# Kernel tuning notes

Hardware: AMD Instinct MI355X
Metric: run time of the kernel (lower is better)

The kernel has to match this reference:

```python
import jax, jax.numpy as jnp
import numpy as np

NEG_SLOPE = 0.2  # PyG GATConv default


def add_self_loops(edge_index, num_nodes):
    loops = jnp.arange(num_nodes, dtype=edge_index.dtype)
    return jnp.concatenate([edge_index, jnp.stack([loops, loops])], axis=1)


def gat_conv(x, edge_index, W, att_src, att_dst, bias, heads, out_ch, concat):
    # x: [N, F_in]; edge_index: [2, E] with row0=src(j), row1=dst(i)
    N = x.shape[0]
    xl = (x @ W).reshape(N, heads, out_ch)              # [N, H, C]
    src, dst = edge_index[0], edge_index[1]
    a_src = jnp.einsum('nhc,hc->nh', xl, att_src)        # [N, H]
    a_dst = jnp.einsum('nhc,hc->nh', xl, att_dst)        # [N, H]
    alpha = jax.nn.leaky_relu(a_src[src] + a_dst[dst], NEG_SLOPE)  # [E, H]
    # segment softmax over incoming edges of each dst node
    m = jax.ops.segment_max(alpha, dst, num_segments=N)  # [N, H]
    e = jnp.exp(alpha - m[dst])
    denom = jax.ops.segment_sum(e, dst, num_segments=N)
    coef = e / (denom[dst] + 1e-16)                      # [E, H]
    msg = xl[src] * coef[..., None]                      # [E, H, C]
    out = jax.ops.segment_sum(msg, dst, num_segments=N)  # [N, H, C]
    out = out.reshape(N, heads * out_ch) if concat else out.mean(axis=1)
    return out + bias


def setup_inputs() -> dict:
    key = jax.random.key(0)
    ks = jax.random.split(key, 12)
    N, E = 50000, 800000
    nfeat, nhid, nheads, nclass = 512, 8, 8, 16
    hid = nhid * nheads  # 64
    s1 = 1.0 / np.sqrt(nfeat)
    s2 = 1.0 / np.sqrt(hid)
    return {
        'x': jax.random.normal(ks[0], (N, nfeat), jnp.float32),
        'edge_index': jax.random.randint(ks[1], (2, E), 0, N, jnp.int64 if jax.config.jax_enable_x64 else jnp.int32),
        'W1': jax.random.uniform(ks[2], (nfeat, hid), jnp.float32, -s1, s1),
        'att_src1': jax.random.uniform(ks[3], (nheads, nhid), jnp.float32, -s2, s2),
        'att_dst1': jax.random.uniform(ks[4], (nheads, nhid), jnp.float32, -s2, s2),
        'bias1': jnp.zeros((hid,), jnp.float32),
        'W2': jax.random.uniform(ks[5], (hid, nclass), jnp.float32, -s2, s2),
        'att_src2': jax.random.uniform(ks[6], (1, nclass), jnp.float32, -0.25, 0.25),
        'att_dst2': jax.random.uniform(ks[7], (1, nclass), jnp.float32, -0.25, 0.25),
        'bias2': jnp.zeros((nclass,), jnp.float32),
    }


def reference(x, edge_index, W1, att_src1, att_dst1, bias1, W2, att_src2, att_dst2, bias2):
    N = x.shape[0]
    ei = add_self_loops(edge_index, N)
    # dropout layers are identity at inference
    h = gat_conv(x, ei, W1, att_src1, att_dst1, bias1, heads=8, out_ch=8, concat=True)
    o = gat_conv(h, ei, W2, att_src2, att_dst2, bias2, heads=1, out_ch=16, concat=True)
    o = jax.nn.elu(o)
    return jax.nn.log_softmax(o, axis=1)
```

## Files before the change

### kernel.cpp

```cpp
#include <hip/hip_runtime.h>
#include <math.h>

#define NEG_SLOPE 0.2f

typedef short short8 __attribute__((ext_vector_type(8)));
typedef float floatx4 __attribute__((ext_vector_type(4)));

static __device__ __forceinline__ float bf2f(unsigned short u) {
  return __uint_as_float(((unsigned int)u) << 16);
}
static __device__ __forceinline__ unsigned short f2bf(float f) {
  unsigned int u = __float_as_uint(f);
  u = (u + 0x7fffu + ((u >> 16) & 1u)) >> 16;
  return (unsigned short)u;
}
static __device__ __forceinline__ unsigned int pack2(float a, float b) {
  return (unsigned int)f2bf(a) | ((unsigned int)f2bf(b) << 16);
}

__global__ void init_misc(const float* __restrict__ W1, unsigned short* __restrict__ W1t,
                          int* __restrict__ deg, int N) {
  int b = blockIdx.x;
  if (b < 128) {
    int i = b * 256 + threadIdx.x;
    int k = i >> 6, c = i & 63;
    W1t[c * 512 + k] = f2bf(W1[i]);
  } else {
    int n = (b - 128) * 256 + threadIdx.x;
    if (n < N) deg[n] = 1;
  }
}

__global__ __launch_bounds__(256) void gemm1_mfma(const float* __restrict__ A,
                                                  const unsigned short* __restrict__ W1t,
                                                  const float* __restrict__ att_src,
                                                  const float* __restrict__ att_dst,
                                                  unsigned short* __restrict__ xlb,
                                                  float* __restrict__ a_src,
                                                  float* __restrict__ a_dst, int M) {
  __shared__ unsigned short As[64 * 72];
  __shared__ unsigned short Bs[64 * 72];
  int tid = threadIdx.x;
  int w = tid >> 6, lane = tid & 63;
  int q = lane >> 4, cl = lane & 15;
  int row0 = blockIdx.x << 6;
  floatx4 acc[4] = {};

  int sr = tid >> 2;
  int skq = (tid & 3) << 4;
  int arow = row0 + sr;
  bool okA = arow < M;
  const float* Aptr = A + (size_t)arow * 512 + skq;
  const unsigned short* Bptr = W1t + sr * 512 + skq;
  unsigned short* AsW = As + sr * 72 + skq;
  unsigned short* BsW = Bs + sr * 72 + skq;

  float4 ca0 = make_float4(0.f, 0.f, 0.f, 0.f), ca1 = ca0, ca2 = ca0, ca3 = ca0;
  uint4 cb0, cb1;
  if (okA) {
    ca0 = *(const float4*)(Aptr);
    ca1 = *(const float4*)(Aptr + 4);
    ca2 = *(const float4*)(Aptr + 8);
    ca3 = *(const float4*)(Aptr + 12);
  }
  cb0 = *(const uint4*)(Bptr);
  cb1 = *(const uint4*)(Bptr + 8);

#pragma unroll
  for (int k0 = 0; k0 < 512; k0 += 64) {
    __syncthreads();
    uint4 a0, a1;
    a0.x = pack2(ca0.x, ca0.y); a0.y = pack2(ca0.z, ca0.w);
    a0.z = pack2(ca1.x, ca1.y); a0.w = pack2(ca1.z, ca1.w);
    a1.x = pack2(ca2.x, ca2.y); a1.y = pack2(ca2.z, ca2.w);
    a1.z = pack2(ca3.x, ca3.y); a1.w = pack2(ca3.z, ca3.w);
    *(uint4*)(AsW) = a0;
    *(uint4*)(AsW + 8) = a1;
    *(uint4*)(BsW) = cb0;
    *(uint4*)(BsW + 8) = cb1;
    __syncthreads();
    if (k0 < 448) {
      ca0 = make_float4(0.f, 0.f, 0.f, 0.f); ca1 = ca0; ca2 = ca0; ca3 = ca0;
      if (okA) {
        ca0 = *(const float4*)(Aptr + k0 + 64);
        ca1 = *(const float4*)(Aptr + k0 + 68);
        ca2 = *(const float4*)(Aptr + k0 + 72);
        ca3 = *(const float4*)(Aptr + k0 + 76);
      }
      cb0 = *(const uint4*)(Bptr + k0 + 64);
      cb1 = *(const uint4*)(Bptr + k0 + 72);
    }
#pragma unroll
    for (int kk = 0; kk < 2; ++kk) {
      short8 af = *(const short8*)(As + (w * 16 + cl) * 72 + kk * 32 + q * 8);
#pragma unroll
      for (int t = 0; t < 4; ++t) {
        short8 bf = *(const short8*)(Bs + (t * 16 + cl) * 72 + kk * 32 + q * 8);
        acc[t] = __builtin_amdgcn_mfma_f32_16x16x32_bf16(af, bf, acc[t], 0, 0, 0);
      }
    }
  }

  float asv[4], adv[4];
#pragma unroll
  for (int t = 0; t < 4; ++t) {
    asv[t] = att_src[t * 16 + cl];
    adv[t] = att_dst[t * 16 + cl];
  }
#pragma unroll
  for (int reg = 0; reg < 4; ++reg) {
    int r = row0 + w * 16 + q * 4 + reg;
    bool ok = r < M;
#pragma unroll
    for (int t = 0; t < 4; ++t) {
      float v = acc[t][reg];
      if (ok) xlb[(size_t)r * 64 + t * 16 + cl] = f2bf(v);
      float ps = v * asv[t];
      float pd = v * adv[t];
      ps += __shfl_xor(ps, 1); pd += __shfl_xor(pd, 1);
      ps += __shfl_xor(ps, 2); pd += __shfl_xor(pd, 2);
      ps += __shfl_xor(ps, 4); pd += __shfl_xor(pd, 4);
      if (ok && (cl & 7) == 0) {
        int h = t * 2 + (cl >> 3);
        a_src[r * 8 + h] = ps;
        a_dst[r * 8 + h] = pd;
      }
    }
  }
}

__global__ __launch_bounds__(256) void deg_hist_sliced(const int* __restrict__ ei,
                                                       int* __restrict__ deg,
                                                       int E, int N, int ipc) {
  int slice = blockIdx.x & 7;
  int chunk = blockIdx.x >> 3;
  int lo = (int)(((long long)slice * N) >> 3);
  int hi = (int)(((long long)(slice + 1) * N) >> 3);
  int beg = chunk * ipc;
  int end = min(beg + ipc, E);
  for (int i = beg + threadIdx.x; i < end; i += 256) {
    int d = ei[E + i];
    if (d >= lo && d < hi) atomicAdd(&deg[d], 1);
  }
}

__global__ __launch_bounds__(256) void partial_sums(const int* __restrict__ deg,
                                                    int* __restrict__ partials, int N) {
  __shared__ int ws[4];
  int base = blockIdx.x * 512;
  int tid = threadIdx.x;
  int i0 = base + tid * 2;
  int s = 0;
  if (i0 < N) s += deg[i0];
  if (i0 + 1 < N) s += deg[i0 + 1];
#pragma unroll
  for (int off = 32; off >= 1; off >>= 1) s += __shfl_xor(s, off, 64);
  if ((tid & 63) == 0) ws[tid >> 6] = s;
  __syncthreads();
  if (tid == 0) partials[blockIdx.x] = ws[0] + ws[1] + ws[2] + ws[3];
}

__global__ __launch_bounds__(256) void scan_partials(const int* __restrict__ partials,
                                                     int* __restrict__ blockoff,
                                                     int* __restrict__ rowptr, int nb, int N) {
  __shared__ int sums[256];
  int tid = threadIdx.x;
  int chunk = (nb + 255) >> 8;
  int start = tid * chunk, end = min(start + chunk, nb);
  int s = 0;
  for (int i = start; i < end; ++i) s += partials[i];
  sums[tid] = s;
  __syncthreads();
  for (int off = 1; off < 256; off <<= 1) {
    int t = (tid >= off) ? sums[tid - off] : 0;
    __syncthreads();
    sums[tid] += t;
    __syncthreads();
  }
  int run = (tid == 0) ? 0 : sums[tid - 1];
  for (int i = start; i < end; ++i) {
    blockoff[i] = run;
    run += partials[i];
  }
  if (tid == 255) rowptr[N] = sums[255];
}

__global__ __launch_bounds__(256) void scan_blocks(const int* __restrict__ deg,
                                                   const int* __restrict__ blockoff,
                                                   int* __restrict__ rowptr,
                                                   int* __restrict__ cursor, int N) {
  __shared__ int wavesum[4];
  int base = blockIdx.x * 512;
  int tid = threadIdx.x;
  int lane = tid & 63, wv = tid >> 6;
  int i0 = base + tid * 2;
  int d0 = (i0 < N) ? deg[i0] : 0;
  int d1 = (i0 + 1 < N) ? deg[i0 + 1] : 0;
  int s = d0 + d1;
  int v = s;
#pragma unroll
  for (int off = 1; off < 64; off <<= 1) {
    int t = __shfl_up(v, off, 64);
    if (lane >= off) v += t;
  }
  if (lane == 63) wavesum[wv] = v;
  __syncthreads();
  int woff = 0;
  for (int w = 0; w < wv; ++w) woff += wavesum[w];
  int excl = v - s + woff + blockoff[blockIdx.x];
  if (i0 < N) { rowptr[i0] = excl; cursor[i0] = excl; }
  if (i0 + 1 < N) { rowptr[i0 + 1] = excl + d0; cursor[i0 + 1] = excl + d0; }
}

__global__ __launch_bounds__(256) void scatter_sliced(const int* __restrict__ ei,
                                                      int* __restrict__ cursor,
                                                      int* __restrict__ srcs,
                                                      int E, int N, int ipc) {
  int slice = blockIdx.x & 7;
  int chunk = blockIdx.x >> 3;
  int lo = (int)(((long long)slice * N) >> 3);
  int hi = (int)(((long long)(slice + 1) * N) >> 3);
  int total = E + N;
  int beg = chunk * ipc;
  int end = min(beg + ipc, total);
  for (int i = beg + threadIdx.x; i < end; i += 256) {
    int d = (i < E) ? ei[E + i] : (i - E);
    if (d >= lo && d < hi) {
      int s = (i < E) ? ei[i] : d;
      int pos = atomicAdd(&cursor[d], 1);
      srcs[pos] = s;
    }
  }
}

__global__ __launch_bounds__(256) void agg1_csr(const int* __restrict__ rowptr,
                                                const int* __restrict__ srcs,
                                                const float* __restrict__ a_src,
                                                const float* __restrict__ a_dst,
                                                const unsigned short* __restrict__ xlb,
                                                float* __restrict__ agg1, int N) {
  int wave = (blockIdx.x * blockDim.x + threadIdx.x) >> 6;
  int lane = threadIdx.x & 63;
  if (wave >= N) return;
  int half = lane >> 5;
  int j = lane & 31;
  int h = j >> 2;
  int beg = rowptr[wave], end = rowptr[wave + 1];
  float ad = a_dst[wave * 8 + h];
  float den = 0.f, acc0 = 0.f, acc1 = 0.f;
  int p = beg;
  for (; p + 4 <= end; p += 4) {
    int sA = srcs[p + half];
    int sB = srcs[p + 2 + half];
    float aA = a_src[sA * 8 + h] + ad;
    float aB = a_src[sB * 8 + h] + ad;
    ushort2 xA = *(const ushort2*)(xlb + (size_t)sA * 64 + 2 * j);
    ushort2 xB = *(const ushort2*)(xlb + (size_t)sB * 64 + 2 * j);
    aA = aA >= 0.f ? aA : NEG_SLOPE * aA;
    aB = aB >= 0.f ? aB : NEG_SLOPE * aB;
    float wA = __expf(aA), wB = __expf(aB);
    den += wA + wB;
    acc0 += wA * bf2f(xA.x) + wB * bf2f(xB.x);
    acc1 += wA * bf2f(xA.y) + wB * bf2f(xB.y);
  }
  for (; p < end; p += 2) {
    int idx = p + half;
    if (idx < end) {
      int s = srcs[idx];
      float a = a_src[s * 8 + h] + ad;
      ushort2 x = *(const ushort2*)(xlb + (size_t)s * 64 + 2 * j);
      a = a >= 0.f ? a : NEG_SLOPE * a;
      float w = __expf(a);
      den += w;
      acc0 += w * bf2f(x.x);
      acc1 += w * bf2f(x.y);
    }
  }
  den += __shfl_xor(den, 32);
  acc0 += __shfl_xor(acc0, 32);
  acc1 += __shfl_xor(acc1, 32);
  if (half == 0) {
    float inv = 1.f / (den + 1e-16f);
    *(float2*)(agg1 + (size_t)wave * 64 + 2 * j) = make_float2(acc0 * inv, acc1 * inv);
  }
}

__global__ __launch_bounds__(256) void gemm2_prep(const float* __restrict__ agg1,
                                                  const float* __restrict__ bias1,
                                                  const float* __restrict__ W2,
                                                  const float* __restrict__ att_src2,
                                                  const float* __restrict__ att_dst2,
                                                  float* __restrict__ xl2,
                                                  float* __restrict__ a_src2,
                                                  float* __restrict__ a_dst2, int N) {
  __shared__ float hs[16 * 68];
  int tid = threadIdx.x;
  int n0 = blockIdx.x << 4;
  {
    int node = tid >> 4;
    int off = (tid & 15) << 2;
    int nn = n0 + node;
    float4 v = make_float4(0.f, 0.f, 0.f, 0.f);
    if (nn < N) {
      v = *(const float4*)(agg1 + (size_t)nn * 64 + off);
      float4 b = *(const float4*)(bias1 + off);
      v.x += b.x; v.y += b.y; v.z += b.z; v.w += b.w;
    }
    *(float4*)(hs + node * 68 + off) = v;
  }
  __syncthreads();
  int t = tid >> 4, c = tid & 15;
  int n = n0 + t;
  if (n >= N) return;
  float sum = 0.f;
#pragma unroll
  for (int k = 0; k < 64; ++k) sum += hs[t * 68 + k] * W2[k * 16 + c];
  xl2[(size_t)n * 16 + c] = sum;
  float ps = sum * att_src2[c];
  float pd = sum * att_dst2[c];
#pragma unroll
  for (int w = 8; w >= 1; w >>= 1) {
    ps += __shfl_xor(ps, w, 16);
    pd += __shfl_xor(pd, w, 16);
  }
  if (c == 0) {
    a_src2[n] = ps;
    a_dst2[n] = pd;
  }
}

__global__ __launch_bounds__(256) void agg2_fin(const int* __restrict__ rowptr,
                                                const int* __restrict__ srcs,
                                                const float* __restrict__ a_src2,
                                                const float* __restrict__ a_dst2,
                                                const float* __restrict__ xl2,
                                                const float* __restrict__ bias2,
                                                float* __restrict__ out, int N) {
  int t = blockIdx.x * blockDim.x + threadIdx.x;
  int node = t >> 4;
  int c = t & 15;
  if (node >= N) return;
  int beg = rowptr[node], end = rowptr[node + 1];
  float ad = a_dst2[node];
  float den = 0.f, acc = 0.f;
  int p = beg;
  for (; p + 4 <= end; p += 4) {
    int s0 = srcs[p], s1 = srcs[p + 1], s2 = srcs[p + 2], s3 = srcs[p + 3];
    float a0 = a_src2[s0], a1 = a_src2[s1], a2 = a_src2[s2], a3 = a_src2[s3];
    float x0 = xl2[(size_t)s0 * 16 + c], x1 = xl2[(size_t)s1 * 16 + c];
    float x2 = xl2[(size_t)s2 * 16 + c], x3 = xl2[(size_t)s3 * 16 + c];
    a0 += ad; a1 += ad; a2 += ad; a3 += ad;
    a0 = a0 >= 0.f ? a0 : NEG_SLOPE * a0;
    a1 = a1 >= 0.f ? a1 : NEG_SLOPE * a1;
    a2 = a2 >= 0.f ? a2 : NEG_SLOPE * a2;
    a3 = a3 >= 0.f ? a3 : NEG_SLOPE * a3;
    float w0 = __expf(a0), w1 = __expf(a1), w2 = __expf(a2), w3 = __expf(a3);
    den += (w0 + w1) + (w2 + w3);
    acc += w0 * x0 + w1 * x1 + w2 * x2 + w3 * x3;
  }
  for (; p < end; ++p) {
    int s = srcs[p];
    float a = a_src2[s] + ad;
    a = a >= 0.f ? a : NEG_SLOPE * a;
    float w = __expf(a);
    den += w;
    acc += w * xl2[(size_t)s * 16 + c];
  }
  float o = acc / (den + 1e-16f) + bias2[c];
  o = o > 0.f ? o : expm1f(o);
  float mx = o;
#pragma unroll
  for (int w = 8; w >= 1; w >>= 1) mx = fmaxf(mx, __shfl_xor(mx, w, 16));
  float e = __expf(o - mx);
  float ssum = e;
#pragma unroll
  for (int w = 8; w >= 1; w >>= 1) ssum += __shfl_xor(ssum, w, 16);
  out[(size_t)node * 16 + c] = o - mx - logf(ssum);
}

extern "C" void kernel_launch(void* const* d_in, const int* in_sizes, int n_in,
                              void* d_out, int out_size, void* d_ws, size_t ws_size,
                              hipStream_t stream) {
  const float* x        = (const float*)d_in[0];
  const int*   ei       = (const int*)d_in[1];
  const float* W1       = (const float*)d_in[2];
  const float* att_src1 = (const float*)d_in[3];
  const float* att_dst1 = (const float*)d_in[4];
  const float* bias1    = (const float*)d_in[5];
  const float* W2       = (const float*)d_in[6];
  const float* att_src2 = (const float*)d_in[7];
  const float* att_dst2 = (const float*)d_in[8];
  const float* bias2    = (const float*)d_in[9];
  float* out = (float*)d_out;

  int N = in_sizes[0] / 512;
  int E = in_sizes[1] / 2;
  int nb = (N + 511) / 512;

  char* ws = (char*)d_ws;
  unsigned short* xlb = (unsigned short*)ws;        ws += (size_t)N * 64 * 2;
  unsigned short* W1t = (unsigned short*)ws;        ws += (size_t)512 * 64 * 2;
  float* a_src1 = (float*)ws;                       ws += (size_t)N * 8 * 4;
  float* a_dst1 = (float*)ws;                       ws += (size_t)N * 8 * 4;
  float* agg1   = (float*)ws;                       ws += (size_t)N * 64 * 4;
  float* xl2    = (float*)ws;                       ws += (size_t)N * 16 * 4;
  float* a_src2 = (float*)ws;                       ws += (size_t)N * 4;
  float* a_dst2 = (float*)ws;                       ws += (size_t)N * 4;
  int* deg      = (int*)ws;                         ws += (size_t)N * 4;
  int* rowptr   = (int*)ws;                         ws += (size_t)(N + 1) * 4;
  int* cursor   = (int*)ws;                         ws += (size_t)N * 4;
  int* srcs     = (int*)ws;                         ws += (size_t)(E + N) * 4;
  int* partials = (int*)ws;                         ws += (size_t)nb * 4;
  int* blockoff = (int*)ws;                         ws += (size_t)nb * 4;

  init_misc<<<128 + (N + 255) / 256, 256, 0, stream>>>(W1, W1t, deg, N);

  const int NCHUNK = 256;
  int ipc_h = (E + NCHUNK - 1) / NCHUNK;
  int ipc_s = (E + N + NCHUNK - 1) / NCHUNK;
  deg_hist_sliced<<<NCHUNK * 8, 256, 0, stream>>>(ei, deg, E, N, ipc_h);
  partial_sums<<<nb, 256, 0, stream>>>(deg, partials, N);
  scan_partials<<<1, 256, 0, stream>>>(partials, blockoff, rowptr, nb, N);
  scan_blocks<<<nb, 256, 0, stream>>>(deg, blockoff, rowptr, cursor, N);
  scatter_sliced<<<NCHUNK * 8, 256, 0, stream>>>(ei, cursor, srcs, E, N, ipc_s);

  gemm1_mfma<<<(N + 63) / 64, 256, 0, stream>>>(x, W1t, att_src1, att_dst1,
                                                xlb, a_src1, a_dst1, N);
  agg1_csr<<<((size_t)N * 64 + 255) / 256, 256, 0, stream>>>(rowptr, srcs, a_src1, a_dst1,
                                                             xlb, agg1, N);

  gemm2_prep<<<(N + 15) / 16, 256, 0, stream>>>(agg1, bias1, W2, att_src2, att_dst2,
                                                xl2, a_src2, a_dst2, N);
  agg2_fin<<<((size_t)N * 16 + 255) / 256, 256, 0, stream>>>(rowptr, srcs, a_src2, a_dst2,
                                                             xl2, bias2, out, N);
}
```

Before: 325.2 us.

## Fuse degree histogram into GEMM1, single-block scan, fuse agg1 with layer-2 projection

The degree histogram now runs as extra blocks of the GEMM1 launch, so the two independent jobs overlap. The three-kernel prefix scan is replaced by one 1024-thread block that loops over the degree array. Layer-1 aggregation is fused with the layer-2 projection, which removes the agg1 intermediate and its global round trip. Both gather loops are software-pipelined with prefetched source indices. The single-block scan serialises a small amount of work, and the fused aggregation kernel adds shared memory and a per-block W2 load.

```diff
diff --git a/kernel.cpp b/kernel.cpp
--- a/kernel.cpp
+++ b/kernel.cpp
@@ -31,15 +31,32 @@
   }
 }
 
-__global__ __launch_bounds__(256) void gemm1_mfma(const float* __restrict__ A,
+__global__ __launch_bounds__(256) void gemm1_hist(const float* __restrict__ A,
                                                   const unsigned short* __restrict__ W1t,
                                                   const float* __restrict__ att_src,
                                                   const float* __restrict__ att_dst,
                                                   unsigned short* __restrict__ xlb,
                                                   float* __restrict__ a_src,
-                                                  float* __restrict__ a_dst, int M) {
+                                                  float* __restrict__ a_dst, int M,
+                                                  const int* __restrict__ ei,
+                                                  int* __restrict__ deg, int E,
+                                                  int ipc, int G1) {
   __shared__ unsigned short As[64 * 72];
   __shared__ unsigned short Bs[64 * 72];
+  if ((int)blockIdx.x >= G1) {
+    int b = blockIdx.x - G1;
+    int slice = b & 7;
+    int chunk = b >> 3;
+    int lo = (int)(((long long)slice * M) >> 3);
+    int hi = (int)(((long long)(slice + 1) * M) >> 3);
+    int beg = chunk * ipc;
+    int end = min(beg + ipc, E);
+    for (int i = beg + threadIdx.x; i < end; i += 256) {
+      int d = ei[E + i];
+      if (d >= lo && d < hi) atomicAdd(&deg[d], 1);
+    }
+    return;
+  }
   int tid = threadIdx.x;
   int w = tid >> 6, lane = tid & 63;
   int q = lane >> 4, cl = lane & 15;
@@ -129,87 +146,62 @@
   }
 }
 
-__global__ __launch_bounds__(256) void deg_hist_sliced(const int* __restrict__ ei,
-                                                       int* __restrict__ deg,
-                                                       int E, int N, int ipc) {
-  int slice = blockIdx.x & 7;
-  int chunk = blockIdx.x >> 3;
-  int lo = (int)(((long long)slice * N) >> 3);
-  int hi = (int)(((long long)(slice + 1) * N) >> 3);
-  int beg = chunk * ipc;
-  int end = min(beg + ipc, E);
-  for (int i = beg + threadIdx.x; i < end; i += 256) {
-    int d = ei[E + i];
-    if (d >= lo && d < hi) atomicAdd(&deg[d], 1);
-  }
-}
-
-__global__ __launch_bounds__(256) void partial_sums(const int* __restrict__ deg,
-                                                    int* __restrict__ partials, int N) {
-  __shared__ int ws[4];
-  int base = blockIdx.x * 512;
-  int tid = threadIdx.x;
-  int i0 = base + tid * 2;
-  int s = 0;
-  if (i0 < N) s += deg[i0];
-  if (i0 + 1 < N) s += deg[i0 + 1];
-#pragma unroll
-  for (int off = 32; off >= 1; off >>= 1) s += __shfl_xor(s, off, 64);
-  if ((tid & 63) == 0) ws[tid >> 6] = s;
-  __syncthreads();
-  if (tid == 0) partials[blockIdx.x] = ws[0] + ws[1] + ws[2] + ws[3];
-}
-
-__global__ __launch_bounds__(256) void scan_partials(const int* __restrict__ partials,
-                                                     int* __restrict__ blockoff,
-                                                     int* __restrict__ rowptr, int nb, int N) {
-  __shared__ int sums[256];
-  int tid = threadIdx.x;
-  int chunk = (nb + 255) >> 8;
-  int start = tid * chunk, end = min(start + chunk, nb);
-  int s = 0;
-  for (int i = start; i < end; ++i) s += partials[i];
-  sums[tid] = s;
-  __syncthreads();
-  for (int off = 1; off < 256; off <<= 1) {
-    int t = (tid >= off) ? sums[tid - off] : 0;
-    __syncthreads();
-    sums[tid] += t;
-    __syncthreads();
-  }
-  int run = (tid == 0) ? 0 : sums[tid - 1];
-  for (int i = start; i < end; ++i) {
-    blockoff[i] = run;
-    run += partials[i];
-  }
-  if (tid == 255) rowptr[N] = sums[255];
-}
-
-__global__ __launch_bounds__(256) void scan_blocks(const int* __restrict__ deg,
-                                                   const int* __restrict__ blockoff,
-                                                   int* __restrict__ rowptr,
-                                                   int* __restrict__ cursor, int N) {
-  __shared__ int wavesum[4];
-  int base = blockIdx.x * 512;
+__global__ __launch_bounds__(1024) void scan_single(const int* __restrict__ deg,
+                                                    int* __restrict__ rowptr,
+                                                    int* __restrict__ cursor, int N) {
+  __shared__ int wsum[16];
   int tid = threadIdx.x;
   int lane = tid & 63, wv = tid >> 6;
-  int i0 = base + tid * 2;
-  int d0 = (i0 < N) ? deg[i0] : 0;
-  int d1 = (i0 + 1 < N) ? deg[i0 + 1] : 0;
-  int s = d0 + d1;
-  int v = s;
-#pragma unroll
-  for (int off = 1; off < 64; off <<= 1) {
-    int t = __shfl_up(v, off, 64);
-    if (lane >= off) v += t;
-  }
-  if (lane == 63) wavesum[wv] = v;
-  __syncthreads();
-  int woff = 0;
-  for (int w = 0; w < wv; ++w) woff += wavesum[w];
-  int excl = v - s + woff + blockoff[blockIdx.x];
-  if (i0 < N) { rowptr[i0] = excl; cursor[i0] = excl; }
-  if (i0 + 1 < N) { rowptr[i0 + 1] = excl + d0; cursor[i0 + 1] = excl + d0; }
+  int carry = 0;
+  for (int base = 0; base < N; base += 8192) {
+    int i0 = base + tid * 8;
+    int d[8];
+    if (i0 + 8 <= N) {
+      int4 a = *(const int4*)(deg + i0);
+      int4 b = *(const int4*)(deg + i0 + 4);
+      d[0] = a.x; d[1] = a.y; d[2] = a.z; d[3] = a.w;
+      d[4] = b.x; d[5] = b.y; d[6] = b.z; d[7] = b.w;
+    } else {
+#pragma unroll
+      for (int k = 0; k < 8; ++k) d[k] = (i0 + k < N) ? deg[i0 + k] : 0;
+    }
+    int e[8];
+    e[0] = d[0];
+#pragma unroll
+    for (int k = 1; k < 8; ++k) e[k] = e[k - 1] + d[k];
+    int tot = e[7];
+    int v = tot;
+#pragma unroll
+    for (int off = 1; off < 64; off <<= 1) {
+      int t = __shfl_up(v, off, 64);
+      if (lane >= off) v += t;
+    }
+    if (lane == 63) wsum[wv] = v;
+    __syncthreads();
+    int woff = carry;
+    for (int w = 0; w < wv; ++w) woff += wsum[w];
+    int excl = woff + v - tot;
+    int r[8];
+    r[0] = excl;
+#pragma unroll
+    for (int k = 1; k < 8; ++k) r[k] = excl + e[k - 1];
+    if (i0 + 8 <= N) {
+      *(int4*)(rowptr + i0)     = make_int4(r[0], r[1], r[2], r[3]);
+      *(int4*)(rowptr + i0 + 4) = make_int4(r[4], r[5], r[6], r[7]);
+      *(int4*)(cursor + i0)     = make_int4(r[0], r[1], r[2], r[3]);
+      *(int4*)(cursor + i0 + 4) = make_int4(r[4], r[5], r[6], r[7]);
+    } else {
+#pragma unroll
+      for (int k = 0; k < 8; ++k)
+        if (i0 + k < N) { rowptr[i0 + k] = r[k]; cursor[i0 + k] = r[k]; }
+    }
+    int bt = 0;
+#pragma unroll
+    for (int w = 0; w < 16; ++w) bt += wsum[w];
+    carry += bt;
+    __syncthreads();
+  }
+  if (tid == 0) rowptr[N] = carry;
 }
 
 __global__ __launch_bounds__(256) void scatter_sliced(const int* __restrict__ ei,
@@ -233,59 +225,11 @@
   }
 }
 
-__global__ __launch_bounds__(256) void agg1_csr(const int* __restrict__ rowptr,
-                                                const int* __restrict__ srcs,
-                                                const float* __restrict__ a_src,
-                                                const float* __restrict__ a_dst,
-                                                const unsigned short* __restrict__ xlb,
-                                                float* __restrict__ agg1, int N) {
-  int wave = (blockIdx.x * blockDim.x + threadIdx.x) >> 6;
-  int lane = threadIdx.x & 63;
-  if (wave >= N) return;
-  int half = lane >> 5;
-  int j = lane & 31;
-  int h = j >> 2;
-  int beg = rowptr[wave], end = rowptr[wave + 1];
-  float ad = a_dst[wave * 8 + h];
-  float den = 0.f, acc0 = 0.f, acc1 = 0.f;
-  int p = beg;
-  for (; p + 4 <= end; p += 4) {
-    int sA = srcs[p + half];
-    int sB = srcs[p + 2 + half];
-    float aA = a_src[sA * 8 + h] + ad;
-    float aB = a_src[sB * 8 + h] + ad;
-    ushort2 xA = *(const ushort2*)(xlb + (size_t)sA * 64 + 2 * j);
-    ushort2 xB = *(const ushort2*)(xlb + (size_t)sB * 64 + 2 * j);
-    aA = aA >= 0.f ? aA : NEG_SLOPE * aA;
-    aB = aB >= 0.f ? aB : NEG_SLOPE * aB;
-    float wA = __expf(aA), wB = __expf(aB);
-    den += wA + wB;
-    acc0 += wA * bf2f(xA.x) + wB * bf2f(xB.x);
-    acc1 += wA * bf2f(xA.y) + wB * bf2f(xB.y);
-  }
-  for (; p < end; p += 2) {
-    int idx = p + half;
-    if (idx < end) {
-      int s = srcs[idx];
-      float a = a_src[s * 8 + h] + ad;
-      ushort2 x = *(const ushort2*)(xlb + (size_t)s * 64 + 2 * j);
-      a = a >= 0.f ? a : NEG_SLOPE * a;
-      float w = __expf(a);
-      den += w;
-      acc0 += w * bf2f(x.x);
-      acc1 += w * bf2f(x.y);
-    }
-  }
-  den += __shfl_xor(den, 32);
-  acc0 += __shfl_xor(acc0, 32);
-  acc1 += __shfl_xor(acc1, 32);
-  if (half == 0) {
-    float inv = 1.f / (den + 1e-16f);
-    *(float2*)(agg1 + (size_t)wave * 64 + 2 * j) = make_float2(acc0 * inv, acc1 * inv);
-  }
-}
-
-__global__ __launch_bounds__(256) void gemm2_prep(const float* __restrict__ agg1,
+__global__ __launch_bounds__(256) void agg1_fused(const int* __restrict__ rowptr,
+                                                  const int* __restrict__ srcs,
+                                                  const float* __restrict__ a_src,
+                                                  const float* __restrict__ a_dst,
+                                                  const unsigned short* __restrict__ xlb,
                                                   const float* __restrict__ bias1,
                                                   const float* __restrict__ W2,
                                                   const float* __restrict__ att_src2,
@@ -293,39 +237,85 @@
                                                   float* __restrict__ xl2,
                                                   float* __restrict__ a_src2,
                                                   float* __restrict__ a_dst2, int N) {
-  __shared__ float hs[16 * 68];
+  __shared__ float W2s[64 * 16];
+  __shared__ float hsm[4][64];
   int tid = threadIdx.x;
-  int n0 = blockIdx.x << 4;
-  {
-    int node = tid >> 4;
-    int off = (tid & 15) << 2;
-    int nn = n0 + node;
-    float4 v = make_float4(0.f, 0.f, 0.f, 0.f);
-    if (nn < N) {
-      v = *(const float4*)(agg1 + (size_t)nn * 64 + off);
-      float4 b = *(const float4*)(bias1 + off);
-      v.x += b.x; v.y += b.y; v.z += b.z; v.w += b.w;
-    }
-    *(float4*)(hs + node * 68 + off) = v;
-  }
+  W2s[tid]       = W2[tid];
+  W2s[tid + 256] = W2[tid + 256];
+  W2s[tid + 512] = W2[tid + 512];
+  W2s[tid + 768] = W2[tid + 768];
   __syncthreads();
-  int t = tid >> 4, c = tid & 15;
-  int n = n0 + t;
-  if (n >= N) return;
-  float sum = 0.f;
-#pragma unroll
-  for (int k = 0; k < 64; ++k) sum += hs[t * 68 + k] * W2[k * 16 + c];
-  xl2[(size_t)n * 16 + c] = sum;
-  float ps = sum * att_src2[c];
-  float pd = sum * att_dst2[c];
-#pragma unroll
-  for (int w = 8; w >= 1; w >>= 1) {
-    ps += __shfl_xor(ps, w, 16);
-    pd += __shfl_xor(pd, w, 16);
-  }
-  if (c == 0) {
-    a_src2[n] = ps;
-    a_dst2[n] = pd;
+
+  int wv = tid >> 6, lane = tid & 63;
+  int node = (blockIdx.x << 2) + wv;
+  if (node >= N) return;
+  int half = lane >> 5;
+  int j = lane & 31;
+  int h = j >> 2;
+  int beg = rowptr[node], end = rowptr[node + 1];
+  float ad = a_dst[node * 8 + h];
+  float den = 0.f, acc0 = 0.f, acc1 = 0.f;
+
+  int p = beg + half;
+  bool v0 = p < end, v1 = p + 2 < end, v2 = p + 4 < end, v3 = p + 6 < end;
+  int s0 = srcs[v0 ? p : beg];
+  int s1 = srcs[v1 ? p + 2 : beg];
+  int s2 = srcs[v2 ? p + 4 : beg];
+  int s3 = srcs[v3 ? p + 6 : beg];
+  while (v0) {
+    int np = p + 8;
+    bool u0 = np < end, u1 = np + 2 < end, u2 = np + 4 < end, u3 = np + 6 < end;
+    int t0 = srcs[u0 ? np : beg];
+    int t1 = srcs[u1 ? np + 2 : beg];
+    int t2 = srcs[u2 ? np + 4 : beg];
+    int t3 = srcs[u3 ? np + 6 : beg];
+    float a0 = a_src[s0 * 8 + h] + ad;
+    float a1 = a_src[s1 * 8 + h] + ad;
+    float a2 = a_src[s2 * 8 + h] + ad;
+    float a3 = a_src[s3 * 8 + h] + ad;
+    ushort2 x0 = *(const ushort2*)(xlb + (size_t)s0 * 64 + 2 * j);
+    ushort2 x1 = *(const ushort2*)(xlb + (size_t)s1 * 64 + 2 * j);
+    ushort2 x2 = *(const ushort2*)(xlb + (size_t)s2 * 64 + 2 * j);
+    ushort2 x3 = *(const ushort2*)(xlb + (size_t)s3 * 64 + 2 * j);
+    a0 = a0 >= 0.f ? a0 : NEG_SLOPE * a0;
+    a1 = a1 >= 0.f ? a1 : NEG_SLOPE * a1;
+    a2 = a2 >= 0.f ? a2 : NEG_SLOPE * a2;
+    a3 = a3 >= 0.f ? a3 : NEG_SLOPE * a3;
+    float w0 = v0 ? __expf(a0) : 0.f;
+    float w1 = v1 ? __expf(a1) : 0.f;
+    float w2 = v2 ? __expf(a2) : 0.f;
+    float w3 = v3 ? __expf(a3) : 0.f;
+    den += (w0 + w1) + (w2 + w3);
+    acc0 += w0 * bf2f(x0.x) + w1 * bf2f(x1.x) + w2 * bf2f(x2.x) + w3 * bf2f(x3.x);
+    acc1 += w0 * bf2f(x0.y) + w1 * bf2f(x1.y) + w2 * bf2f(x2.y) + w3 * bf2f(x3.y);
+    p = np;
+    s0 = t0; s1 = t1; s2 = t2; s3 = t3;
+    v0 = u0; v1 = u1; v2 = u2; v3 = u3;
+  }
+  den  += __shfl_xor(den, 32);
+  acc0 += __shfl_xor(acc0, 32);
+  acc1 += __shfl_xor(acc1, 32);
+  float inv = 1.f / (den + 1e-16f);
+  float2 bv = *(const float2*)(bias1 + 2 * j);
+  float h0 = acc0 * inv + bv.x;
+  float h1 = acc1 * inv + bv.y;
+  if (half == 0) {
+    hsm[wv][2 * j]     = h0;
+    hsm[wv][2 * j + 1] = h1;
+  }
+  if (lane < 16) {
+    float sum = 0.f;
+#pragma unroll
+    for (int k = 0; k < 64; ++k) sum += hsm[wv][k] * W2s[k * 16 + lane];
+    xl2[(size_t)node * 16 + lane] = sum;
+    float ps = sum * att_src2[lane];
+    float pd = sum * att_dst2[lane];
+#pragma unroll
+    for (int w = 8; w >= 1; w >>= 1) {
+      ps += __shfl_xor(ps, w, 16);
+      pd += __shfl_xor(pd, w, 16);
+    }
+    if (lane == 0) { a_src2[node] = ps; a_dst2[node] = pd; }
   }
 }
 
@@ -344,27 +334,35 @@
   float ad = a_dst2[node];
   float den = 0.f, acc = 0.f;
   int p = beg;
-  for (; p + 4 <= end; p += 4) {
-    int s0 = srcs[p], s1 = srcs[p + 1], s2 = srcs[p + 2], s3 = srcs[p + 3];
-    float a0 = a_src2[s0], a1 = a_src2[s1], a2 = a_src2[s2], a3 = a_src2[s3];
+  bool v0 = true, v1 = p + 1 < end, v2 = p + 2 < end, v3 = p + 3 < end;
+  int s0 = srcs[p];
+  int s1 = srcs[v1 ? p + 1 : beg];
+  int s2 = srcs[v2 ? p + 2 : beg];
+  int s3 = srcs[v3 ? p + 3 : beg];
+  while (v0) {
+    int np = p + 4;
+    bool u0 = np < end, u1 = np + 1 < end, u2 = np + 2 < end, u3 = np + 3 < end;
+    int t0 = srcs[u0 ? np : beg];
+    int t1 = srcs[u1 ? np + 1 : beg];
+    int t2 = srcs[u2 ? np + 2 : beg];
+    int t3 = srcs[u3 ? np + 3 : beg];
+    float a0 = a_src2[s0] + ad, a1 = a_src2[s1] + ad;
+    float a2 = a_src2[s2] + ad, a3 = a_src2[s3] + ad;
     float x0 = xl2[(size_t)s0 * 16 + c], x1 = xl2[(size_t)s1 * 16 + c];
     float x2 = xl2[(size_t)s2 * 16 + c], x3 = xl2[(size_t)s3 * 16 + c];
-    a0 += ad; a1 += ad; a2 += ad; a3 += ad;
     a0 = a0 >= 0.f ? a0 : NEG_SLOPE * a0;
     a1 = a1 >= 0.f ? a1 : NEG_SLOPE * a1;
     a2 = a2 >= 0.f ? a2 : NEG_SLOPE * a2;
     a3 = a3 >= 0.f ? a3 : NEG_SLOPE * a3;
-    float w0 = __expf(a0), w1 = __expf(a1), w2 = __expf(a2), w3 = __expf(a3);
+    float w0 = v0 ? __expf(a0) : 0.f;
+    float w1 = v1 ? __expf(a1) : 0.f;
+    float w2 = v2 ? __expf(a2) : 0.f;
+    float w3 = v3 ? __expf(a3) : 0.f;
     den += (w0 + w1) + (w2 + w3);
     acc += w0 * x0 + w1 * x1 + w2 * x2 + w3 * x3;
-  }
-  for (; p < end; ++p) {
-    int s = srcs[p];
-    float a = a_src2[s] + ad;
-    a = a >= 0.f ? a : NEG_SLOPE * a;
-    float w = __expf(a);
-    den += w;
-    acc += w * xl2[(size_t)s * 16 + c];
+    p = np;
+    s0 = t0; s1 = t1; s2 = t2; s3 = t3;
+    v0 = u0; v1 = u1; v2 = u2; v3 = u3;
   }
   float o = acc / (den + 1e-16f) + bias2[c];
   o = o > 0.f ? o : expm1f(o);
@@ -377,6 +375,8 @@
   for (int w = 8; w >= 1; w >>= 1) ssum += __shfl_xor(ssum, w, 16);
   out[(size_t)node * 16 + c] = o - mx - logf(ssum);
 }
+
+static inline size_t rnd16(size_t x) { return (x + 15) & ~(size_t)15; }
 
 extern "C" void kernel_launch(void* const* d_in, const int* in_sizes, int n_in,
                               void* d_out, int out_size, void* d_ws, size_t ws_size,
@@ -395,42 +395,34 @@
 
   int N = in_sizes[0] / 512;
   int E = in_sizes[1] / 2;
-  int nb = (N + 511) / 512;
 
   char* ws = (char*)d_ws;
-  unsigned short* xlb = (unsigned short*)ws;        ws += (size_t)N * 64 * 2;
-  unsigned short* W1t = (unsigned short*)ws;        ws += (size_t)512 * 64 * 2;
-  float* a_src1 = (float*)ws;                       ws += (size_t)N * 8 * 4;
-  float* a_dst1 = (float*)ws;                       ws += (size_t)N * 8 * 4;
-  float* agg1   = (float*)ws;                       ws += (size_t)N * 64 * 4;
-  float* xl2    = (float*)ws;                       ws += (size_t)N * 16 * 4;
-  float* a_src2 = (float*)ws;                       ws += (size_t)N * 4;
-  float* a_dst2 = (float*)ws;                       ws += (size_t)N * 4;
-  int* deg      = (int*)ws;                         ws += (size_t)N * 4;
-  int* rowptr   = (int*)ws;                         ws += (size_t)(N + 1) * 4;
-  int* cursor   = (int*)ws;                         ws += (size_t)N * 4;
-  int* srcs     = (int*)ws;                         ws += (size_t)(E + N) * 4;
-  int* partials = (int*)ws;                         ws += (size_t)nb * 4;
-  int* blockoff = (int*)ws;                         ws += (size_t)nb * 4;
-
-  init_misc<<<128 + (N + 255) / 256, 256, 0, stream>>>(W1, W1t, deg, N);
+  unsigned short* xlb = (unsigned short*)ws;  ws += rnd16((size_t)N * 64 * 2);
+  unsigned short* W1t = (unsigned short*)ws;  ws += rnd16((size_t)512 * 64 * 2);
+  float* a_src1 = (float*)ws;                 ws += rnd16((size_t)N * 8 * 4);
+  float* a_dst1 = (float*)ws;                 ws += rnd16((size_t)N * 8 * 4);
+  float* xl2    = (float*)ws;                 ws += rnd16((size_t)N * 16 * 4);
+  float* a_src2 = (float*)ws;                 ws += rnd16((size_t)N * 4);
+  float* a_dst2 = (float*)ws;                 ws += rnd16((size_t)N * 4);
+  int* deg      = (int*)ws;                   ws += rnd16((size_t)N * 4);
+  int* rowptr   = (int*)ws;                   ws += rnd16((size_t)(N + 1) * 4);
+  int* cursor   = (int*)ws;                   ws += rnd16((size_t)N * 4);
+  int* srcs     = (int*)ws;                   ws += rnd16((size_t)(E + N) * 4);
 
   const int NCHUNK = 256;
+  int G1 = (N + 63) / 64;
   int ipc_h = (E + NCHUNK - 1) / NCHUNK;
   int ipc_s = (E + N + NCHUNK - 1) / NCHUNK;
-  deg_hist_sliced<<<NCHUNK * 8, 256, 0, stream>>>(ei, deg, E, N, ipc_h);
-  partial_sums<<<nb, 256, 0, stream>>>(deg, partials, N);
-  scan_partials<<<1, 256, 0, stream>>>(partials, blockoff, rowptr, nb, N);
-  scan_blocks<<<nb, 256, 0, stream>>>(deg, blockoff, rowptr, cursor, N);
+
+  init_misc<<<128 + (N + 255) / 256, 256, 0, stream>>>(W1, W1t, deg, N);
+  gemm1_hist<<<G1 + NCHUNK * 8, 256, 0, stream>>>(x, W1t, att_src1, att_dst1,
+                                                  xlb, a_src1, a_dst1, N,
+                                                  ei, deg, E, ipc_h, G1);
+  scan_single<<<1, 1024, 0, stream>>>(deg, rowptr, cursor, N);
   scatter_sliced<<<NCHUNK * 8, 256, 0, stream>>>(ei, cursor, srcs, E, N, ipc_s);
-
-  gemm1_mfma<<<(N + 63) / 64, 256, 0, stream>>>(x, W1t, att_src1, att_dst1,
-                                                xlb, a_src1, a_dst1, N);
-  agg1_csr<<<((size_t)N * 64 + 255) / 256, 256, 0, stream>>>(rowptr, srcs, a_src1, a_dst1,
-                                                             xlb, agg1, N);
-
-  gemm2_prep<<<(N + 15) / 16, 256, 0, stream>>>(agg1, bias1, W2, att_src2, att_dst2,
-                                                xl2, a_src2, a_dst2, N);
+  agg1_fused<<<(N + 3) / 4, 256, 0, stream>>>(rowptr, srcs, a_src1, a_dst1, xlb,
+                                              bias1, W2, att_src2, att_dst2,
+                                              xl2, a_src2, a_dst2, N);
   agg2_fin<<<((size_t)N * 16 + 255) / 256, 256, 0, stream>>>(rowptr, srcs, a_src2, a_dst2,
                                                              xl2, bias2, out, N);
 }
```

After: 311.5 us. -4.2%, faster.
